# Performance work log

Hardware: AMD Instinct MI355X
Metric: run time of the kernel (lower is better)

## Reference

```python
import jax, jax.numpy as jnp
import numpy as np

N, F_IN, HID, HEADS, CLASSES, E = 50000, 256, 64, 4, 64, 800000
NEG_SLOPE = 0.2


def _glorot(key, shape):
    fan = shape[0] + shape[-1]
    return jax.random.normal(key, shape, jnp.float32) * jnp.sqrt(2.0 / fan)


def setup_inputs() -> dict:
    key = jax.random.key(0)
    ks = jax.random.split(key, 12)
    x = jax.random.normal(ks[0], (N, F_IN), jnp.float32)
    edge_index = jax.random.randint(ks[1], (2, E), 0, N, jnp.int32)
    d = {"x": x, "edge_index": edge_index}
    dims = [(F_IN, HID), (HEADS * HID, HID), (HEADS * HID, CLASSES)]
    k = 2
    for li, (din, dout) in enumerate(dims, start=1):
        d[f"W{li}"] = _glorot(ks[k], (din, HEADS * dout)); k += 1
        d[f"a_src{li}"] = _glorot(ks[k], (HEADS, dout)); k += 1
        d[f"a_dst{li}"] = _glorot(ks[k], (HEADS, dout)); k += 1
        bdim = HEADS * dout if li < 3 else dout
        d[f"b{li}"] = jnp.zeros((bdim,), jnp.float32)
    return d


def _gat_layer(x, src, dst, W, a_src, a_dst, b, out_dim, concat):
    n = x.shape[0]
    h = (x @ W).reshape(n, HEADS, out_dim)            # [N,H,D]
    al_s = jnp.einsum("nhd,hd->nh", h, a_src)         # [N,H]
    al_d = jnp.einsum("nhd,hd->nh", h, a_dst)
    logits = jax.nn.leaky_relu(al_s[src] + al_d[dst], NEG_SLOPE)  # [E,H]
    # segment softmax over destination nodes (self-loops guarantee non-empty)
    m = jax.ops.segment_max(logits, dst, num_segments=n)
    e = jnp.exp(logits - m[dst])
    denom = jax.ops.segment_sum(e, dst, num_segments=n)
    att = e / denom[dst]                              # [E,H]
    msg = h[src] * att[:, :, None]                    # [E,H,D]
    out = jax.ops.segment_sum(msg, dst, num_segments=n)
    out = out.reshape(n, HEADS * out_dim) if concat else out.mean(axis=1)
    return out + b


def reference(x, edge_index, W1, a_src1, a_dst1, b1, W2, a_src2, a_dst2, b2,
              W3, a_src3, a_dst3, b3):
    loop = jnp.arange(N, dtype=edge_index.dtype)
    src = jnp.concatenate([edge_index[0], loop])
    dst = jnp.concatenate([edge_index[1], loop])
    h = _gat_layer(x, src, dst, W1, a_src1, a_dst1, b1, HID, True)
    h = jax.nn.elu(h)  # dropout is identity in eval mode
    h = _gat_layer(h, src, dst, W2, a_src2, a_dst2, b2, HID, True)
    h = jax.nn.elu(h)
    h = _gat_layer(h, src, dst, W3, a_src3, a_dst3, b3, CLASSES, False)
    return jax.nn.log_softmax(h, axis=-1)
```

## Files before the change

### kernel.cpp

```cpp
#include <hip/hip_runtime.h>
#include <stdint.h>

typedef __bf16 bf16x8 __attribute__((ext_vector_type(8)));
typedef float f32x4 __attribute__((ext_vector_type(4)));
typedef unsigned short u16x8 __attribute__((ext_vector_type(8)));

__device__ __forceinline__ unsigned short f2bf(float f){
  union { float f; unsigned u; } c; c.f = f;
  unsigned u = c.u;
  unsigned r = u + 0x7FFFu + ((u >> 16) & 1u);
  return (unsigned short)(r >> 16);
}

__global__ void k_prehist(const int* __restrict__ ei, int E, int Nn, int* __restrict__ counts,
                          const float* __restrict__ W1, const float* __restrict__ W2,
                          const float* __restrict__ W3, unsigned short* __restrict__ p1,
                          unsigned short* __restrict__ p2, unsigned short* __restrict__ p3){
  int b = blockIdx.x;
  if (b < 96){
    int t = b*256 + threadIdx.x;
    int which = t >> 13, li = t & 8191;
    const float* W = (which == 0) ? W1 : (which == 1) ? W2 : W3;
    unsigned short* P = (which == 0) ? p1 : (which == 1) ? p2 : p3;
    int l = li & 63, c = (li >> 6) & 3, kb = (li >> 8) & 7, w = li >> 11;
    int r = l & 15, kg = l >> 4;
    int col = w*64 + c*16 + r;
    int k0 = kb*32 + kg*8;
    unsigned short v[8];
    #pragma unroll
    for (int j = 0; j < 8; ++j) v[j] = f2bf(W[(size_t)(k0 + j)*256 + col]);
    *reinterpret_cast<uint4*>(P + (size_t)li*8) = *reinterpret_cast<const uint4*>(v);
  } else {
    int total = E + Nn;
    for (int e = (b - 96)*256 + threadIdx.x; e < total; e += (gridDim.x - 96)*256){
      int d = (e < E) ? ei[E + e] : (e - E);
      atomicAdd(&counts[d], 1);
    }
  }
}

__global__ __launch_bounds__(1024) void k_scan1(const int* __restrict__ counts, int* __restrict__ rowptr,
                                                int* __restrict__ bsum, int n){
  __shared__ int wsum[17];
  int tid = threadIdx.x, lane = tid & 63, wid = tid >> 6;
  int i = blockIdx.x*1024 + tid;
  int v = (i < n) ? counts[i] : 0;
  int iv = v;
  #pragma unroll
  for (int off = 1; off < 64; off <<= 1){
    int t = __shfl_up(iv, off, 64);
    if (lane >= off) iv += t;
  }
  if (lane == 63) wsum[wid] = iv;
  __syncthreads();
  if (tid == 0){
    int run = 0;
    for (int w = 0; w < 16; ++w){ int t = wsum[w]; wsum[w] = run; run += t; }
    wsum[16] = run;
  }
  __syncthreads();
  if (i < n) rowptr[i + 1] = iv + wsum[wid];
  if (tid == 0) bsum[blockIdx.x] = wsum[16];
}

__global__ __launch_bounds__(1024) void k_scan2(int* __restrict__ bsum, int nb){
  __shared__ int wsum[17];
  int tid = threadIdx.x, lane = tid & 63, wid = tid >> 6;
  int v = (tid < nb) ? bsum[tid] : 0;
  int iv = v;
  #pragma unroll
  for (int off = 1; off < 64; off <<= 1){
    int t = __shfl_up(iv, off, 64);
    if (lane >= off) iv += t;
  }
  if (lane == 63) wsum[wid] = iv;
  __syncthreads();
  if (tid == 0){
    int run = 0;
    for (int w = 0; w < 16; ++w){ int t = wsum[w]; wsum[w] = run; run += t; }
  }
  __syncthreads();
  if (tid < nb) bsum[tid] = iv + wsum[wid] - v;
}

__global__ void k_scan3(int* __restrict__ rowptr, const int* __restrict__ bsum,
                        const int* __restrict__ counts, int* __restrict__ cursor, int n){
  int i = blockIdx.x*blockDim.x + threadIdx.x;
  if (i == 0) rowptr[0] = 0;
  if (i < n){
    int v = rowptr[i + 1] + bsum[i >> 10];
    rowptr[i + 1] = v;
    cursor[i] = v - counts[i];
  }
}

__global__ void k_scatter(const int* __restrict__ ei, int E, int Nn,
                          int* __restrict__ cursor, int* __restrict__ srcs){
  int total = E + Nn;
  for (int e = blockIdx.x*blockDim.x + threadIdx.x; e < total; e += gridDim.x*blockDim.x){
    int s, d;
    if (e < E){ s = ei[e]; d = ei[E + e]; } else { s = d = e - E; }
    int pos = atomicAdd(&cursor[d], 1);
    srcs[pos] = s;
  }
}

template<bool AF32>
__global__ __launch_bounds__(256) void k_gemm7(const void* __restrict__ Av,
                                               const unsigned short* __restrict__ Bp,
                                               const float* __restrict__ asrc,
                                               const float* __restrict__ adst,
                                               unsigned short* __restrict__ H,
                                               float* __restrict__ als,
                                               float* __restrict__ ald,
                                               int Nn){
  __shared__ unsigned short As[32][264];
  int tid = threadIdx.x;
  int w = tid >> 6, lane = tid & 63;
  int r = lane & 15, kg = lane >> 4;
  int row0 = blockIdx.x * 32;

  const unsigned short* a16 = (const unsigned short*)Av;
  const float*          a32 = (const float*)Av;
  const unsigned short* bpw = Bp + ((size_t)w << 14);

  bf16x8 bf0[4], bf1[4];
  #pragma unroll
  for (int c = 0; c < 4; ++c)
    bf0[c] = *reinterpret_cast<const bf16x8*>(bpw + ((size_t)(c*64 + lane))*8);

  #pragma unroll
  for (int it = 0; it < 4; ++it){
    int li = it*256 + tid;
    int rr = li >> 5, c16 = li & 31;
    int gr = row0 + rr; if (gr >= Nn) gr = Nn - 1;
    if (AF32){
      const float* ap = a32 + (size_t)gr*256 + c16*8;
      float4 v0 = *reinterpret_cast<const float4*>(ap);
      float4 v1 = *reinterpret_cast<const float4*>(ap + 4);
      union { uint4 q; unsigned short s[8]; } u;
      u.s[0]=f2bf(v0.x); u.s[1]=f2bf(v0.y); u.s[2]=f2bf(v0.z); u.s[3]=f2bf(v0.w);
      u.s[4]=f2bf(v1.x); u.s[5]=f2bf(v1.y); u.s[6]=f2bf(v1.z); u.s[7]=f2bf(v1.w);
      *reinterpret_cast<uint4*>(&As[rr][c16*8]) = u.q;
    } else {
      uint4 v = *reinterpret_cast<const uint4*>(a16 + (size_t)gr*256 + c16*8);
      *reinterpret_cast<uint4*>(&As[rr][c16*8]) = v;
    }
  }
  __syncthreads();

  f32x4 acc[2][4] = {};
  #pragma unroll
  for (int kb = 0; kb < 8; ++kb){
    if (kb < 7){
      if (kb & 1){
        #pragma unroll
        for (int c = 0; c < 4; ++c)
          bf0[c] = *reinterpret_cast<const bf16x8*>(bpw + ((size_t)(((kb+1)*4 + c)*64 + lane))*8);
      } else {
        #pragma unroll
        for (int c = 0; c < 4; ++c)
          bf1[c] = *reinterpret_cast<const bf16x8*>(bpw + ((size_t)(((kb+1)*4 + c)*64 + lane))*8);
      }
    }
    bf16x8 a0 = *reinterpret_cast<const bf16x8*>(&As[r][kg*8 + kb*32]);
    bf16x8 a1 = *reinterpret_cast<const bf16x8*>(&As[16 + r][kg*8 + kb*32]);
    if (kb & 1){
      #pragma unroll
      for (int c = 0; c < 4; ++c){
        acc[0][c] = __builtin_amdgcn_mfma_f32_16x16x32_bf16(bf1[c], a0, acc[0][c], 0, 0, 0);
        acc[1][c] = __builtin_amdgcn_mfma_f32_16x16x32_bf16(bf1[c], a1, acc[1][c], 0, 0, 0);
      }
    } else {
      #pragma unroll
      for (int c = 0; c < 4; ++c){
        acc[0][c] = __builtin_amdgcn_mfma_f32_16x16x32_bf16(bf0[c], a0, acc[0][c], 0, 0, 0);
        acc[1][c] = __builtin_amdgcn_mfma_f32_16x16x32_bf16(bf0[c], a1, acc[1][c], 0, 0, 0);
      }
    }
  }

  #pragma unroll
  for (int n = 0; n < 2; ++n){
    int row = row0 + n*16 + r;
    if (row < Nn){
      #pragma unroll
      for (int c = 0; c < 4; ++c){
        ushort4 pk;
        pk.x = f2bf(acc[n][c][0]); pk.y = f2bf(acc[n][c][1]);
        pk.z = f2bf(acc[n][c][2]); pk.w = f2bf(acc[n][c][3]);
        *reinterpret_cast<ushort4*>(H + (size_t)row*256 + w*64 + c*16 + kg*4) = pk;
      }
    }
  }

  float4 as4[4], ad4[4];
  #pragma unroll
  for (int c = 0; c < 4; ++c){
    as4[c] = *reinterpret_cast<const float4*>(asrc + w*64 + c*16 + kg*4);
    ad4[c] = *reinterpret_cast<const float4*>(adst + w*64 + c*16 + kg*4);
  }
  #pragma unroll
  for (int n = 0; n < 2; ++n){
    float ps = 0.f, pd = 0.f;
    #pragma unroll
    for (int c = 0; c < 4; ++c){
      ps += acc[n][c][0]*as4[c].x + acc[n][c][1]*as4[c].y
          + acc[n][c][2]*as4[c].z + acc[n][c][3]*as4[c].w;
      pd += acc[n][c][0]*ad4[c].x + acc[n][c][1]*ad4[c].y
          + acc[n][c][2]*ad4[c].z + acc[n][c][3]*ad4[c].w;
    }
    ps += __shfl_xor(ps, 16, 64); ps += __shfl_xor(ps, 32, 64);
    pd += __shfl_xor(pd, 16, 64); pd += __shfl_xor(pd, 32, 64);
    int row = row0 + n*16 + r;
    if (kg == 0 && row < Nn){
      als[row*4 + w] = ps;
      ald[row*4 + w] = pd;
    }
  }
}

template<int MODE>
__global__ void k_gather3(const unsigned short* __restrict__ Hm, const int* __restrict__ rowptr,
                          const int* __restrict__ srcs, const float* __restrict__ als,
                          const float* __restrict__ ald, const float* __restrict__ bias,
                          unsigned short* __restrict__ actout, float* __restrict__ finalout, int Nn){
  int gid = blockIdx.x*blockDim.x + threadIdx.x;
  int node = gid >> 6, lane = gid & 63;
  if (node >= Nn) return;
  int half = lane >> 5;
  int l32  = lane & 31;
  int fbase = l32 * 8;
  int hd = l32 >> 3;
  unsigned voff_feat = (unsigned)(l32 * 16);

  int beg = rowptr[node], deg = rowptr[node + 1] - beg;
  float4 adv = *reinterpret_cast<const float4*>(ald + (size_t)node*4);
  float aldh = (hd == 0) ? adv.x : (hd == 1) ? adv.y : (hd == 2) ? adv.z : adv.w;

  float acc[4][8];
  #pragma unroll
  for (int u = 0; u < 4; ++u)
    #pragma unroll
    for (int i = 0; i < 8; ++i) acc[u][i] = 0.f;
  float sw = 0.f;

  const char* Hb = (const char*)Hm;
  const char* Ab = (const char*)als;

  for (int cb = 0; cb < deg; cb += 64){
    int chunk = min(64, deg - cb);
    int mysrc = (cb + lane < deg) ? srcs[beg + cb + lane] : 0;
    int jmax8 = chunk & ~7;
    int j = 0;
    for (; j < jmax8; j += 8){
      #pragma unroll
      for (int u = 0; u < 4; ++u){
        int e0 = j + 2*u;
        int sA = __builtin_amdgcn_readlane(mysrc, e0);
        int sB = __builtin_amdgcn_readlane(mysrc, e0 + 1);
        int sM = half ? sB : sA;
        uint4 hw = *reinterpret_cast<const uint4*>(Hb + (unsigned)sM*512u + voff_feat);
        float av = *reinterpret_cast<const float*>(Ab + ((unsigned)sM << 4) + ((unsigned)hd << 2));
        float l = av + aldh; l = l > 0.f ? l : 0.2f*l;
        float wgt = __expf(l);
        sw += wgt;
        float h0 = __uint_as_float(hw.x << 16);
        float h1 = __uint_as_float(hw.x & 0xffff0000u);
        float h2 = __uint_as_float(hw.y << 16);
        float h3 = __uint_as_float(hw.y & 0xffff0000u);
        float h4 = __uint_as_float(hw.z << 16);
        float h5 = __uint_as_float(hw.z & 0xffff0000u);
        float h6 = __uint_as_float(hw.w << 16);
        float h7 = __uint_as_float(hw.w & 0xffff0000u);
        acc[u][0] = fmaf(wgt, h0, acc[u][0]);
        acc[u][1] = fmaf(wgt, h1, acc[u][1]);
        acc[u][2] = fmaf(wgt, h2, acc[u][2]);
        acc[u][3] = fmaf(wgt, h3, acc[u][3]);
        acc[u][4] = fmaf(wgt, h4, acc[u][4]);
        acc[u][5] = fmaf(wgt, h5, acc[u][5]);
        acc[u][6] = fmaf(wgt, h6, acc[u][6]);
        acc[u][7] = fmaf(wgt, h7, acc[u][7]);
      }
    }
    for (; j < chunk; j += 2){
      int eA = j;
      int eB = (j + 1 < chunk) ? (j + 1) : j;
      int sA = __builtin_amdgcn_readlane(mysrc, eA);
      int sB = __builtin_amdgcn_readlane(mysrc, eB);
      int sM = half ? sB : sA;
      uint4 hw = *reinterpret_cast<const uint4*>(Hb + (unsigned)sM*512u + voff_feat);
      float av = *reinterpret_cast<const float*>(Ab + ((unsigned)sM << 4) + ((unsigned)hd << 2));
      float l = av + aldh; l = l > 0.f ? l : 0.2f*l;
      float wgt = __expf(l);
      if (j + half >= chunk) wgt = 0.f;
      sw += wgt;
      float h0 = __uint_as_float(hw.x << 16);
      float h1 = __uint_as_float(hw.x & 0xffff0000u);
      float h2 = __uint_as_float(hw.y << 16);
      float h3 = __uint_as_float(hw.y & 0xffff0000u);
      float h4 = __uint_as_float(hw.z << 16);
      float h5 = __uint_as_float(hw.z & 0xffff0000u);
      float h6 = __uint_as_float(hw.w << 16);
      float h7 = __uint_as_float(hw.w & 0xffff0000u);
      acc[0][0] = fmaf(wgt, h0, acc[0][0]);
      acc[0][1] = fmaf(wgt, h1, acc[0][1]);
      acc[0][2] = fmaf(wgt, h2, acc[0][2]);
      acc[0][3] = fmaf(wgt, h3, acc[0][3]);
      acc[0][4] = fmaf(wgt, h4, acc[0][4]);
      acc[0][5] = fmaf(wgt, h5, acc[0][5]);
      acc[0][6] = fmaf(wgt, h6, acc[0][6]);
      acc[0][7] = fmaf(wgt, h7, acc[0][7]);
    }
  }

  float accf[8];
  #pragma unroll
  for (int i = 0; i < 8; ++i){
    float t = acc[0][i] + acc[1][i] + acc[2][i] + acc[3][i];
    t += __shfl_xor(t, 32, 64);
    accf[i] = t;
  }
  float s = sw + __shfl_xor(sw, 32, 64);
  float inv = 1.f / s;

  if (MODE == 0){
    if (lane < 32){
      float4 b0 = *reinterpret_cast<const float4*>(bias + fbase);
      float4 b1 = *reinterpret_cast<const float4*>(bias + fbase + 4);
      float o[8];
      o[0] = accf[0]*inv + b0.x; o[1] = accf[1]*inv + b0.y;
      o[2] = accf[2]*inv + b0.z; o[3] = accf[3]*inv + b0.w;
      o[4] = accf[4]*inv + b1.x; o[5] = accf[5]*inv + b1.y;
      o[6] = accf[6]*inv + b1.z; o[7] = accf[7]*inv + b1.w;
      u16x8 pk;
      #pragma unroll
      for (int i = 0; i < 8; ++i){
        float v = o[i];
        v = v > 0.f ? v : __expf(v) - 1.f;
        pk[i] = f2bf(v);
      }
      *reinterpret_cast<u16x8*>(actout + (size_t)node*256 + fbase) = pk;
    }
  } else {
    float v[8];
    #pragma unroll
    for (int i = 0; i < 8; ++i){
      float t = accf[i]*inv;
      t += __shfl_xor(t, 8, 64);
      t += __shfl_xor(t, 16, 64);
      v[i] = t;
    }
    int k = l32 & 7;
    float4 b0 = *reinterpret_cast<const float4*>(bias + k*8);
    float4 b1 = *reinterpret_cast<const float4*>(bias + k*8 + 4);
    v[0] = v[0]*0.25f + b0.x; v[1] = v[1]*0.25f + b0.y;
    v[2] = v[2]*0.25f + b0.z; v[3] = v[3]*0.25f + b0.w;
    v[4] = v[4]*0.25f + b1.x; v[5] = v[5]*0.25f + b1.y;
    v[6] = v[6]*0.25f + b1.z; v[7] = v[7]*0.25f + b1.w;
    float mx = v[0];
    #pragma unroll
    for (int i = 1; i < 8; ++i) mx = fmaxf(mx, v[i]);
    #pragma unroll
    for (int off = 1; off < 8; off <<= 1) mx = fmaxf(mx, __shfl_xor(mx, off, 64));
    float se = 0.f;
    #pragma unroll
    for (int i = 0; i < 8; ++i) se += __expf(v[i] - mx);
    #pragma unroll
    for (int off = 1; off < 8; off <<= 1) se += __shfl_xor(se, off, 64);
    float lse = mx + __logf(se);
    if (lane < 8){
      float4 o0, o1;
      o0.x = v[0]-lse; o0.y = v[1]-lse; o0.z = v[2]-lse; o0.w = v[3]-lse;
      o1.x = v[4]-lse; o1.y = v[5]-lse; o1.z = v[6]-lse; o1.w = v[7]-lse;
      float* dst = finalout + (size_t)node*64 + lane*8;
      *reinterpret_cast<float4*>(dst)     = o0;
      *reinterpret_cast<float4*>(dst + 4) = o1;
    }
  }
}

extern "C" void kernel_launch(void* const* d_in, const int* in_sizes, int n_in,
                              void* d_out, int out_size, void* d_ws, size_t ws_size,
                              hipStream_t stream){
  const float* x     = (const float*)d_in[0];
  const int*   ei    = (const int*)  d_in[1];
  const float* W1    = (const float*)d_in[2];
  const float* asrc1 = (const float*)d_in[3];
  const float* adst1 = (const float*)d_in[4];
  const float* b1    = (const float*)d_in[5];
  const float* W2    = (const float*)d_in[6];
  const float* asrc2 = (const float*)d_in[7];
  const float* adst2 = (const float*)d_in[8];
  const float* b2    = (const float*)d_in[9];
  const float* W3    = (const float*)d_in[10];
  const float* asrc3 = (const float*)d_in[11];
  const float* adst3 = (const float*)d_in[12];
  const float* b3    = (const float*)d_in[13];
  float* out = (float*)d_out;

  int N = in_sizes[0] / 256;
  int E = in_sizes[1] / 2;

  char* p = (char*)d_ws;
  auto carve = [&](size_t bytes){ void* r = (void*)p; p += (bytes + 511) & ~(size_t)511; return r; };
  unsigned short* bufA = (unsigned short*)carve((size_t)N*256*2);
  unsigned short* bufH = (unsigned short*)carve((size_t)N*256*2);
  unsigned short* bufB = (unsigned short*)carve((size_t)N*256*2);
  unsigned short* bp1  = (unsigned short*)carve(256*256*2);
  unsigned short* bp2  = (unsigned short*)carve(256*256*2);
  unsigned short* bp3  = (unsigned short*)carve(256*256*2);
  float* als    = (float*)carve((size_t)N*4*4);
  float* ald    = (float*)carve((size_t)N*4*4);
  int* rowptr   = (int*)carve((size_t)(N+1)*4);
  int* counts   = (int*)carve((size_t)N*4);
  int* cursor   = (int*)carve((size_t)N*4);
  int* bsum     = (int*)carve((size_t)1024*4);
  int* srcs     = (int*)carve((size_t)(E+N)*4);

  hipMemsetAsync(counts, 0, (size_t)N*4, stream);
  k_prehist<<<96 + 2048, 256, 0, stream>>>(ei, E, N, counts, W1, W2, W3, bp1, bp2, bp3);
  int nb = (N + 1023) / 1024;
  k_scan1<<<nb, 1024, 0, stream>>>(counts, rowptr, bsum, N);
  k_scan2<<<1, 1024, 0, stream>>>(bsum, nb);
  k_scan3<<<(N + 255)/256, 256, 0, stream>>>(rowptr, bsum, counts, cursor, N);
  k_scatter<<<2048, 256, 0, stream>>>(ei, E, N, cursor, srcs);

  int gemm_grid  = (N + 31) / 32;
  int nodeblocks = (N*64 + 255)/256;

  k_gemm7<true><<<gemm_grid, 256, 0, stream>>>(x, bp1, asrc1, adst1, bufH, als, ald, N);
  k_gather3<0><<<nodeblocks, 256, 0, stream>>>(bufH, rowptr, srcs, als, ald, b1, bufB, nullptr, N);
  k_gemm7<false><<<gemm_grid, 256, 0, stream>>>(bufB, bp2, asrc2, adst2, bufH, als, ald, N);
  k_gather3<0><<<nodeblocks, 256, 0, stream>>>(bufH, rowptr, srcs, als, ald, b2, bufA, nullptr, N);
  k_gemm7<false><<<gemm_grid, 256, 0, stream>>>(bufA, bp3, asrc3, adst3, bufH, als, ald, N);
  k_gather3<1><<<nodeblocks, 256, 0, stream>>>(bufH, rowptr, srcs, als, ald, b3, nullptr, out, N);
}
```

Baseline: 377.2 us.

## Make GEMM persistent with register-prefetched next A tile overlapping MFMA

Each GEMM block now processes tiles in a grid-stride loop (half as many blocks, two tiles each) and prefetches the next 32-row A tile into registers while MFMAs run on the current tile in LDS. The goal is to hide global-load latency of the activation rows behind compute. In exchange it raises register pressure, which can lower occupancy, and it halves the grid, which may reduce the parallelism available to hide latency.

```diff
diff --git a/kernel.cpp b/kernel.cpp
--- a/kernel.cpp
+++ b/kernel.cpp
@@ -106,117 +106,148 @@
 }
 
 template<bool AF32>
-__global__ __launch_bounds__(256) void k_gemm7(const void* __restrict__ Av,
+__global__ __launch_bounds__(256) void k_gemm8(const void* __restrict__ Av,
                                                const unsigned short* __restrict__ Bp,
                                                const float* __restrict__ asrc,
                                                const float* __restrict__ adst,
                                                unsigned short* __restrict__ H,
                                                float* __restrict__ als,
                                                float* __restrict__ ald,
-                                               int Nn){
+                                               int Nn, int T, int G){
   __shared__ unsigned short As[32][264];
   int tid = threadIdx.x;
   int w = tid >> 6, lane = tid & 63;
   int r = lane & 15, kg = lane >> 4;
-  int row0 = blockIdx.x * 32;
 
   const unsigned short* a16 = (const unsigned short*)Av;
   const float*          a32 = (const float*)Av;
   const unsigned short* bpw = Bp + ((size_t)w << 14);
 
-  bf16x8 bf0[4], bf1[4];
-  #pragma unroll
-  for (int c = 0; c < 4; ++c)
-    bf0[c] = *reinterpret_cast<const bf16x8*>(bpw + ((size_t)(c*64 + lane))*8);
-
-  #pragma unroll
-  for (int it = 0; it < 4; ++it){
-    int li = it*256 + tid;
-    int rr = li >> 5, c16 = li & 31;
-    int gr = row0 + rr; if (gr >= Nn) gr = Nn - 1;
-    if (AF32){
-      const float* ap = a32 + (size_t)gr*256 + c16*8;
-      float4 v0 = *reinterpret_cast<const float4*>(ap);
-      float4 v1 = *reinterpret_cast<const float4*>(ap + 4);
-      union { uint4 q; unsigned short s[8]; } u;
-      u.s[0]=f2bf(v0.x); u.s[1]=f2bf(v0.y); u.s[2]=f2bf(v0.z); u.s[3]=f2bf(v0.w);
-      u.s[4]=f2bf(v1.x); u.s[5]=f2bf(v1.y); u.s[6]=f2bf(v1.z); u.s[7]=f2bf(v1.w);
-      *reinterpret_cast<uint4*>(&As[rr][c16*8]) = u.q;
-    } else {
-      uint4 v = *reinterpret_cast<const uint4*>(a16 + (size_t)gr*256 + c16*8);
-      *reinterpret_cast<uint4*>(&As[rr][c16*8]) = v;
-    }
-  }
-  __syncthreads();
-
-  f32x4 acc[2][4] = {};
-  #pragma unroll
-  for (int kb = 0; kb < 8; ++kb){
-    if (kb < 7){
+  uint4  sreg[4];
+  float4 sregf[4][2];
+
+  auto load_tile = [&](int t){
+    #pragma unroll
+    for (int it = 0; it < 4; ++it){
+      int li = it*256 + tid;
+      int rr = li >> 5, c16 = li & 31;
+      int gr = t*32 + rr; if (gr >= Nn) gr = Nn - 1;
+      if (AF32){
+        const float* ap = a32 + (size_t)gr*256 + c16*8;
+        sregf[it][0] = *reinterpret_cast<const float4*>(ap);
+        sregf[it][1] = *reinterpret_cast<const float4*>(ap + 4);
+      } else {
+        sreg[it] = *reinterpret_cast<const uint4*>(a16 + (size_t)gr*256 + c16*8);
+      }
+    }
+  };
+  auto write_lds = [&](){
+    #pragma unroll
+    for (int it = 0; it < 4; ++it){
+      int li = it*256 + tid;
+      int rr = li >> 5, c16 = li & 31;
+      if (AF32){
+        float4 v0 = sregf[it][0], v1 = sregf[it][1];
+        union { uint4 q; unsigned short s[8]; } u;
+        u.s[0]=f2bf(v0.x); u.s[1]=f2bf(v0.y); u.s[2]=f2bf(v0.z); u.s[3]=f2bf(v0.w);
+        u.s[4]=f2bf(v1.x); u.s[5]=f2bf(v1.y); u.s[6]=f2bf(v1.z); u.s[7]=f2bf(v1.w);
+        *reinterpret_cast<uint4*>(&As[rr][c16*8]) = u.q;
+      } else {
+        *reinterpret_cast<uint4*>(&As[rr][c16*8]) = sreg[it];
+      }
+    }
+  };
+
+  int t = blockIdx.x;
+  if (t >= T) return;
+  load_tile(t);
+
+  for (;;){
+    write_lds();
+    __syncthreads();
+    int tn = t + G;
+    bool more = (tn < T);
+    if (more) load_tile(tn);
+
+    bf16x8 bf0[4], bf1[4];
+    #pragma unroll
+    for (int c = 0; c < 4; ++c)
+      bf0[c] = *reinterpret_cast<const bf16x8*>(bpw + ((size_t)(c*64 + lane))*8);
+
+    f32x4 acc[2][4] = {};
+    #pragma unroll
+    for (int kb = 0; kb < 8; ++kb){
+      if (kb < 7){
+        if (kb & 1){
+          #pragma unroll
+          for (int c = 0; c < 4; ++c)
+            bf0[c] = *reinterpret_cast<const bf16x8*>(bpw + ((size_t)(((kb+1)*4 + c)*64 + lane))*8);
+        } else {
+          #pragma unroll
+          for (int c = 0; c < 4; ++c)
+            bf1[c] = *reinterpret_cast<const bf16x8*>(bpw + ((size_t)(((kb+1)*4 + c)*64 + lane))*8);
+        }
+      }
+      bf16x8 a0 = *reinterpret_cast<const bf16x8*>(&As[r][kg*8 + kb*32]);
+      bf16x8 a1 = *reinterpret_cast<const bf16x8*>(&As[16 + r][kg*8 + kb*32]);
       if (kb & 1){
         #pragma unroll
-        for (int c = 0; c < 4; ++c)
-          bf0[c] = *reinterpret_cast<const bf16x8*>(bpw + ((size_t)(((kb+1)*4 + c)*64 + lane))*8);
+        for (int c = 0; c < 4; ++c){
+          acc[0][c] = __builtin_amdgcn_mfma_f32_16x16x32_bf16(bf1[c], a0, acc[0][c], 0, 0, 0);
+          acc[1][c] = __builtin_amdgcn_mfma_f32_16x16x32_bf16(bf1[c], a1, acc[1][c], 0, 0, 0);
+        }
       } else {
         #pragma unroll
-        for (int c = 0; c < 4; ++c)
-          bf1[c] = *reinterpret_cast<const bf16x8*>(bpw + ((size_t)(((kb+1)*4 + c)*64 + lane))*8);
-      }
-    }
-    bf16x8 a0 = *reinterpret_cast<const bf16x8*>(&As[r][kg*8 + kb*32]);
-    bf16x8 a1 = *reinterpret_cast<const bf16x8*>(&As[16 + r][kg*8 + kb*32]);
-    if (kb & 1){
+        for (int c = 0; c < 4; ++c){
+          acc[0][c] = __builtin_amdgcn_mfma_f32_16x16x32_bf16(bf0[c], a0, acc[0][c], 0, 0, 0);
+          acc[1][c] = __builtin_amdgcn_mfma_f32_16x16x32_bf16(bf0[c], a1, acc[1][c], 0, 0, 0);
+        }
+      }
+    }
+
+    int row0 = t*32;
+    #pragma unroll
+    for (int n = 0; n < 2; ++n){
+      int row = row0 + n*16 + r;
+      if (row < Nn){
+        #pragma unroll
+        for (int c = 0; c < 4; ++c){
+          ushort4 pk;
+          pk.x = f2bf(acc[n][c][0]); pk.y = f2bf(acc[n][c][1]);
+          pk.z = f2bf(acc[n][c][2]); pk.w = f2bf(acc[n][c][3]);
+          *reinterpret_cast<ushort4*>(H + (size_t)row*256 + w*64 + c*16 + kg*4) = pk;
+        }
+      }
+    }
+
+    float4 as4[4], ad4[4];
+    #pragma unroll
+    for (int c = 0; c < 4; ++c){
+      as4[c] = *reinterpret_cast<const float4*>(asrc + w*64 + c*16 + kg*4);
+      ad4[c] = *reinterpret_cast<const float4*>(adst + w*64 + c*16 + kg*4);
+    }
+    #pragma unroll
+    for (int n = 0; n < 2; ++n){
+      float ps = 0.f, pd = 0.f;
       #pragma unroll
       for (int c = 0; c < 4; ++c){
-        acc[0][c] = __builtin_amdgcn_mfma_f32_16x16x32_bf16(bf1[c], a0, acc[0][c], 0, 0, 0);
-        acc[1][c] = __builtin_amdgcn_mfma_f32_16x16x32_bf16(bf1[c], a1, acc[1][c], 0, 0, 0);
-      }
-    } else {
-      #pragma unroll
-      for (int c = 0; c < 4; ++c){
-        acc[0][c] = __builtin_amdgcn_mfma_f32_16x16x32_bf16(bf0[c], a0, acc[0][c], 0, 0, 0);
-        acc[1][c] = __builtin_amdgcn_mfma_f32_16x16x32_bf16(bf0[c], a1, acc[1][c], 0, 0, 0);
-      }
-    }
-  }
-
-  #pragma unroll
-  for (int n = 0; n < 2; ++n){
-    int row = row0 + n*16 + r;
-    if (row < Nn){
-      #pragma unroll
-      for (int c = 0; c < 4; ++c){
-        ushort4 pk;
-        pk.x = f2bf(acc[n][c][0]); pk.y = f2bf(acc[n][c][1]);
-        pk.z = f2bf(acc[n][c][2]); pk.w = f2bf(acc[n][c][3]);
-        *reinterpret_cast<ushort4*>(H + (size_t)row*256 + w*64 + c*16 + kg*4) = pk;
-      }
-    }
-  }
-
-  float4 as4[4], ad4[4];
-  #pragma unroll
-  for (int c = 0; c < 4; ++c){
-    as4[c] = *reinterpret_cast<const float4*>(asrc + w*64 + c*16 + kg*4);
-    ad4[c] = *reinterpret_cast<const float4*>(adst + w*64 + c*16 + kg*4);
-  }
-  #pragma unroll
-  for (int n = 0; n < 2; ++n){
-    float ps = 0.f, pd = 0.f;
-    #pragma unroll
-    for (int c = 0; c < 4; ++c){
-      ps += acc[n][c][0]*as4[c].x + acc[n][c][1]*as4[c].y
-          + acc[n][c][2]*as4[c].z + acc[n][c][3]*as4[c].w;
-      pd += acc[n][c][0]*ad4[c].x + acc[n][c][1]*ad4[c].y
-          + acc[n][c][2]*ad4[c].z + acc[n][c][3]*ad4[c].w;
-    }
-    ps += __shfl_xor(ps, 16, 64); ps += __shfl_xor(ps, 32, 64);
-    pd += __shfl_xor(pd, 16, 64); pd += __shfl_xor(pd, 32, 64);
-    int row = row0 + n*16 + r;
-    if (kg == 0 && row < Nn){
-      als[row*4 + w] = ps;
-      ald[row*4 + w] = pd;
-    }
+        ps += acc[n][c][0]*as4[c].x + acc[n][c][1]*as4[c].y
+            + acc[n][c][2]*as4[c].z + acc[n][c][3]*as4[c].w;
+        pd += acc[n][c][0]*ad4[c].x + acc[n][c][1]*ad4[c].y
+            + acc[n][c][2]*ad4[c].z + acc[n][c][3]*ad4[c].w;
+      }
+      ps += __shfl_xor(ps, 16, 64); ps += __shfl_xor(ps, 32, 64);
+      pd += __shfl_xor(pd, 16, 64); pd += __shfl_xor(pd, 32, 64);
+      int row = row0 + n*16 + r;
+      if (kg == 0 && row < Nn){
+        als[row*4 + w] = ps;
+        ald[row*4 + w] = pd;
+      }
+    }
+
+    if (!more) break;
+    __syncthreads();
+    t = tn;
   }
 }
 
@@ -426,13 +457,14 @@
   k_scan3<<<(N + 255)/256, 256, 0, stream>>>(rowptr, bsum, counts, cursor, N);
   k_scatter<<<2048, 256, 0, stream>>>(ei, E, N, cursor, srcs);
 
-  int gemm_grid  = (N + 31) / 32;
+  int T = (N + 31) / 32;
+  int G = (T + 1) / 2;
   int nodeblocks = (N*64 + 255)/256;
 
-  k_gemm7<true><<<gemm_grid, 256, 0, stream>>>(x, bp1, asrc1, adst1, bufH, als, ald, N);
+  k_gemm8<true><<<G, 256, 0, stream>>>(x, bp1, asrc1, adst1, bufH, als, ald, N, T, G);
   k_gather3<0><<<nodeblocks, 256, 0, stream>>>(bufH, rowptr, srcs, als, ald, b1, bufB, nullptr, N);
-  k_gemm7<false><<<gemm_grid, 256, 0, stream>>>(bufB, bp2, asrc2, adst2, bufH, als, ald, N);
+  k_gemm8<false><<<G, 256, 0, stream>>>(bufB, bp2, asrc2, adst2, bufH, als, ald, N, T, G);
   k_gather3<0><<<nodeblocks, 256, 0, stream>>>(bufH, rowptr, srcs, als, ald, b2, bufA, nullptr, N);
-  k_gemm7<false><<<gemm_grid, 256, 0, stream>>>(bufA, bp3, asrc3, adst3, bufH, als, ald, N);
+  k_gemm8<false><<<G, 256, 0, stream>>>(bufA, bp3, asrc3, adst3, bufH, als, ald, N, T, G);
   k_gather3<1><<<nodeblocks, 256, 0, stream>>>(bufH, rowptr, srcs, als, ald, b3, nullptr, out, N);
 }
```

After: 390.0 us. +3.4%, slower.
